# Optimization experiments

Measured on AMD Instinct MI355X. Metric: run time of the kernel, lower is better.

## Reference

```python
import jax, jax.numpy as jnp
import numpy as np

SQRT_HALF = np.float32(np.sqrt(0.5))
H_AX, W_AX = 2, 3


def _refl_idx(idx, r):
    # symmetric extension with edge repetition (np.pad mode='symmetric'),
    # identical to dtcwt's reflect(idx, -0.5, r-0.5). Static numpy computation.
    idx = np.mod(idx, 2 * r)
    return np.where(idx < r, idx, 2 * r - 1 - idx)


def _filt(X, h, axis):
    # Non-decimating 1-D filtering (dtcwt colfilter/rowfilter): symmetric pad by
    # len(h)//2, true convolution, 'valid' -> output same length as input.
    X = jnp.moveaxis(X, axis, -1)
    m = h.shape[0]
    m2 = m // 2
    L = X.shape[-1]
    Xp = jnp.pad(X, [(0, 0)] * (X.ndim - 1) + [(m2, m2)], mode='symmetric')
    out = sum(h[m - 1 - j] * Xp[..., j:j + L] for j in range(m))  # flip -> convolution
    return jnp.moveaxis(out, -1, axis)


def _dfilt(X, ha, hb, highpass, axis):
    # Decimate-by-2 dual-tree filtering (dtcwt coldfilt/rowdfilt).
    # ha filters one polyphase stream, hb the other; outputs are interleaved.
    X = jnp.moveaxis(X, axis, -1)
    r = X.shape[-1]
    assert r % 4 == 0, 'filtered dim must be a multiple of 4'
    m = ha.shape[0]
    m2 = m // 2
    xe = _refl_idx(np.arange(-m, r + m), r)        # symmetric-extended indices
    t = np.arange(5, r + 2 * m - 2, 4)             # 0-based MATLAB t = 6:4:r+2m-2
    hao, hae = ha[0::2], ha[1::2]
    hbo, hbe = hb[0::2], hb[1::2]

    def cv(rows, f):
        # 'valid' true convolution along gathered (stride-4) sample sequence
        A = X[..., rows]
        Lout = rows.shape[0] - m2 + 1              # == r // 4
        return sum(f[m2 - 1 - j] * A[..., j:j + Lout] for j in range(m2))

    ya = cv(xe[t - 1], hao) + cv(xe[t - 3], hae)
    yb = cv(xe[t], hbo) + cv(xe[t - 2], hbe)
    first, second = (yb, ya) if highpass else (ya, yb)
    Y = jnp.stack([first, second], axis=-1).reshape(X.shape[:-1] + (r // 2,))
    return jnp.moveaxis(Y, -1, axis)


def _q2c(y):
    # quads -> two complex subimages: p = (a+jb)/sqrt2, q = (d-jc)/sqrt2; z = p -/+ q
    a = y[..., 0::2, 0::2]
    b = y[..., 0::2, 1::2]
    c = y[..., 1::2, 0::2]
    d = y[..., 1::2, 1::2]
    z1 = ((a - d) * SQRT_HALF, (b + c) * SQRT_HALF)
    z2 = ((a + d) * SQRT_HALF, (b - c) * SQRT_HALF)
    return z1, z2


def _bands_to_yh(lh, hl, hh):
    # orientation order 15,45,75,105,135,165 degrees; output [N,C,6,H',W',2]
    (r15, i15), (r165, i165) = _q2c(lh)
    (r45, i45), (r135, i135) = _q2c(hh)
    (r75, i75), (r105, i105) = _q2c(hl)
    reals = jnp.stack([r15, r45, r75, r105, r135, r165], axis=2)
    imags = jnp.stack([i15, i45, i75, i105, i135, i165], axis=2)
    return jnp.stack([reals, imags], axis=-1)


def _dtcwt_fwd(x, h0o, h1o, h0a, h0b, h1a, h1b, J=3):
    # Level 1: non-decimating biorthogonal filters
    lo = _filt(x, h0o, W_AX)
    hi = _filt(x, h1o, W_AX)
    ll = _filt(lo, h0o, H_AX)
    yh = [_bands_to_yh(_filt(lo, h1o, H_AX),   # lh
                       _filt(hi, h0o, H_AX),   # hl
                       _filt(hi, h1o, H_AX))]  # hh
    # Levels 2..J: decimating qshift filters
    for _ in range(1, J):
        lo = _dfilt(ll, h0b, h0a, False, W_AX)
        hi = _dfilt(ll, h1b, h1a, True, W_AX)
        ll = _dfilt(lo, h0b, h0a, False, H_AX)
        yh.append(_bands_to_yh(_dfilt(lo, h1b, h1a, True, H_AX),
                               _dfilt(hi, h0b, h0a, False, H_AX),
                               _dfilt(hi, h1b, h1a, True, H_AX)))
    return (ll, *yh)


def setup_inputs() -> dict:
    key = jax.random.key(0)
    ks = jax.random.split(key, 5)
    x = jax.random.normal(ks[0], (4, 16, 512, 512), dtype=jnp.float32)

    def mk(k, n):
        h = jax.random.normal(k, (n,), dtype=jnp.float32)
        return h / jnp.linalg.norm(h)  # unit-norm to keep levels well scaled

    h0o = mk(ks[1], 5)
    h1o = mk(ks[2], 7)
    h0a = mk(ks[3], 10)
    h1a = mk(ks[4], 10)
    h0b = h0a[::-1]  # dual-tree property: tree-b = time-reversed tree-a
    h1b = h1a[::-1]
    return {'x': x, 'h0o': h0o, 'h1o': h1o, 'h0a': h0a, 'h0b': h0b,
            'h1a': h1a, 'h1b': h1b}


def reference(x, h0o, h1o, h0a, h0b, h1a, h1b):
    # Returns (yl, yh_level1, yh_level2, yh_level3)
    return _dtcwt_fwd(x, h0o, h1o, h0a, h0b, h1a, h1b, J=3)
```

## Files before the change

### kernel.cpp

```cpp
#include <hip/hip_runtime.h>

#define S1 512
#define NIMG 64

typedef float f4v __attribute__((ext_vector_type(4)));
typedef float f2v __attribute__((ext_vector_type(2)));

__device__ __forceinline__ int refl(int a, int L) {
    a = (a < 0) ? (-a - 1) : a;
    a = (a >= L) ? (2 * L - 1 - a) : a;
    return a;
}

__device__ __forceinline__ void st_nt_f4(float* p, float a, float b, float c, float d) {
    f4v w = {a, b, c, d};
    __builtin_nontemporal_store(w, (f4v*)p);
}
__device__ __forceinline__ void st_nt_f2(float* p, float a, float b) {
    f2v w = {a, b};
    __builtin_nontemporal_store(w, (f2v*)p);
}

__global__ __launch_bounds__(256) void k_level1(
    const float* __restrict__ x,
    const float* __restrict__ h0o_g, const float* __restrict__ h1o_g,
    float* __restrict__ ll1, float* __restrict__ yh0)
{
    __shared__ float xs[38 * 72];
    __shared__ float lo_s[38 * 68];
    __shared__ float hi_s[38 * 68];

    const int t  = threadIdx.x;
    const int c0 = blockIdx.x * 64;
    const int r0 = blockIdx.y * 64;
    const int n  = blockIdx.z;
    const float* __restrict__ xn  = x   + (size_t)n * (S1 * S1);
    float* __restrict__ lln       = ll1 + (size_t)n * (S1 * S1);
    float* __restrict__ yhn       = yh0 + (size_t)n * (6 * 256 * 256 * 2);

    float f0[5], f1[7];
#pragma unroll
    for (int i = 0; i < 5; ++i) f0[i] = h0o_g[i];
#pragma unroll
    for (int i = 0; i < 7; ++i) f1[i] = h1o_g[i];

    const float SQH = 0.70710678118654752440f;

    for (int h = 0; h < 2; ++h) {
        const int gr0 = r0 + 32 * h - 3;

        for (int l = t; l < 38 * 16; l += 256) {
            int rl = l >> 4, cf = l & 15;
            int ar = refl(gr0 + rl, S1);
            *(float4*)&xs[rl * 72 + 4 + 4 * cf] =
                *(const float4*)&xn[(size_t)ar * S1 + c0 + 4 * cf];
        }
        if (t < 76) {
            int rl = t >> 1, side = t & 1;
            const float* __restrict__ row = &xn[(size_t)refl(gr0 + rl, S1) * S1];
            int xc = side ? 68 : 0;
            int gc = side ? (c0 + 64) : (c0 - 4);
            if (gc >= 0 && gc + 3 < S1) {
                *(float4*)&xs[rl * 72 + xc] = *(const float4*)&row[gc];
            } else {
#pragma unroll
                for (int k = 0; k < 4; ++k)
                    xs[rl * 72 + xc + k] = row[refl(gc + k, S1)];
            }
        }
        __syncthreads();

        for (int l = t; l < 38 * 16; l += 256) {
            int rl = l >> 4, cg = l & 15;
            const float* p = &xs[rl * 72 + 4 * cg];
            float4 va = *(const float4*)p;
            float4 vb = *(const float4*)(p + 4);
            float4 vc = *(const float4*)(p + 8);
            float V[12] = {va.x, va.y, va.z, va.w, vb.x, vb.y, vb.z, vb.w,
                           vc.x, vc.y, vc.z, vc.w};
            float lov[4], hiv[4];
#pragma unroll
            for (int cc = 0; cc < 4; ++cc) {
                lov[cc] = f0[0]*V[cc+6] + f0[1]*V[cc+5] + f0[2]*V[cc+4]
                        + f0[3]*V[cc+3] + f0[4]*V[cc+2];
                hiv[cc] = f1[0]*V[cc+7] + f1[1]*V[cc+6] + f1[2]*V[cc+5]
                        + f1[3]*V[cc+4] + f1[4]*V[cc+3] + f1[5]*V[cc+2]
                        + f1[6]*V[cc+1];
            }
            *(float4*)&lo_s[rl * 68 + 4 * cg] = make_float4(lov[0], lov[1], lov[2], lov[3]);
            *(float4*)&hi_s[rl * 68 + 4 * cg] = make_float4(hiv[0], hiv[1], hiv[2], hiv[3]);
        }
        __syncthreads();

        {
            const int qi = t >> 4, cg = t & 15;
            float4 Lv[8];
            float llv[2][4], lhv[2][4], hlv[2][4], hhv[2][4];

#pragma unroll
            for (int j = 0; j < 8; ++j)
                Lv[j] = *(const float4*)&lo_s[(2 * qi + j) * 68 + 4 * cg];
            {
                const float* L = (const float*)Lv;
#pragma unroll
                for (int cc = 0; cc < 4; ++cc) {
                    float Lc[8];
#pragma unroll
                    for (int j = 0; j < 8; ++j) Lc[j] = L[4 * j + cc];
                    llv[0][cc] = f0[0]*Lc[5] + f0[1]*Lc[4] + f0[2]*Lc[3] + f0[3]*Lc[2] + f0[4]*Lc[1];
                    llv[1][cc] = f0[0]*Lc[6] + f0[1]*Lc[5] + f0[2]*Lc[4] + f0[3]*Lc[3] + f0[4]*Lc[2];
                    lhv[0][cc] = f1[0]*Lc[6] + f1[1]*Lc[5] + f1[2]*Lc[4] + f1[3]*Lc[3]
                               + f1[4]*Lc[2] + f1[5]*Lc[1] + f1[6]*Lc[0];
                    lhv[1][cc] = f1[0]*Lc[7] + f1[1]*Lc[6] + f1[2]*Lc[5] + f1[3]*Lc[4]
                               + f1[4]*Lc[3] + f1[5]*Lc[2] + f1[6]*Lc[1];
                }
            }
#pragma unroll
            for (int j = 0; j < 8; ++j)
                Lv[j] = *(const float4*)&hi_s[(2 * qi + j) * 68 + 4 * cg];
            {
                const float* L = (const float*)Lv;
#pragma unroll
                for (int cc = 0; cc < 4; ++cc) {
                    float Lc[8];
#pragma unroll
                    for (int j = 0; j < 8; ++j) Lc[j] = L[4 * j + cc];
                    hlv[0][cc] = f0[0]*Lc[5] + f0[1]*Lc[4] + f0[2]*Lc[3] + f0[3]*Lc[2] + f0[4]*Lc[1];
                    hlv[1][cc] = f0[0]*Lc[6] + f0[1]*Lc[5] + f0[2]*Lc[4] + f0[3]*Lc[3] + f0[4]*Lc[2];
                    hhv[0][cc] = f1[0]*Lc[6] + f1[1]*Lc[5] + f1[2]*Lc[4] + f1[3]*Lc[3]
                               + f1[4]*Lc[2] + f1[5]*Lc[1] + f1[6]*Lc[0];
                    hhv[1][cc] = f1[0]*Lc[7] + f1[1]*Lc[6] + f1[2]*Lc[5] + f1[3]*Lc[4]
                               + f1[4]*Lc[3] + f1[5]*Lc[2] + f1[6]*Lc[1];
                }
            }

            const int oy = r0 + 32 * h + 2 * qi, ox = c0 + 4 * cg;
            *(float4*)&lln[(size_t)oy * S1 + ox] =
                make_float4(llv[0][0], llv[0][1], llv[0][2], llv[0][3]);
            *(float4*)&lln[(size_t)(oy + 1) * S1 + ox] =
                make_float4(llv[1][0], llv[1][1], llv[1][2], llv[1][3]);

            const int i2 = (r0 >> 1) + 16 * h + qi, j2 = (c0 >> 1) + 2 * cg;
            const size_t bs = 256 * 256 * 2;
            float* __restrict__ p = yhn + ((size_t)i2 * 256 + j2) * 2;
#define ST_Z1(P, X0, X1) st_nt_f4((P), (X0[0]-X1[1])*SQH, (X0[1]+X1[0])*SQH, \
                                       (X0[2]-X1[3])*SQH, (X0[3]+X1[2])*SQH)
#define ST_Z2(P, X0, X1) st_nt_f4((P), (X0[0]+X1[1])*SQH, (X0[1]-X1[0])*SQH, \
                                       (X0[2]+X1[3])*SQH, (X0[3]-X1[2])*SQH)
            ST_Z1(p + 0 * bs, lhv[0], lhv[1]);
            ST_Z1(p + 1 * bs, hhv[0], hhv[1]);
            ST_Z1(p + 2 * bs, hlv[0], hlv[1]);
            ST_Z2(p + 3 * bs, hlv[0], hlv[1]);
            ST_Z2(p + 4 * bs, hhv[0], hhv[1]);
            ST_Z2(p + 5 * bs, lhv[0], lhv[1]);
#undef ST_Z1
#undef ST_Z2
        }
        __syncthreads();
    }
}

__global__ __launch_bounds__(256) void k_dfilt(
    const float* __restrict__ X, const int r,
    const float* __restrict__ h0a_g, const float* __restrict__ h0b_g,
    const float* __restrict__ h1a_g, const float* __restrict__ h1b_g,
    float* __restrict__ llo, float* __restrict__ yh)
{
    __shared__ float Xc[16 * 84];
    __shared__ float lo_s[80 * 36];
    __shared__ float hi_s[80 * 36];

    const int t  = threadIdx.x;
    const int x0 = blockIdx.x * 32;
    const int y0 = blockIdx.y * 32;
    const int n  = blockIdx.z;
    const float* __restrict__ Xn = X + (size_t)n * r * r;
    const int cb = 2 * x0 - 8, rb = 2 * y0 - 8;

    float fa0[10], fb0[10], fa1[10], fb1[10];
#pragma unroll
    for (int i = 0; i < 10; ++i) {
        fa0[i] = h0a_g[i]; fb0[i] = h0b_g[i];
        fa1[i] = h1a_g[i]; fb1[i] = h1b_g[i];
    }

    for (int c = 0; c < 5; ++c) {
        const int rbase = rb + 16 * c;
        {
            int rl = t >> 4, cf = t & 15;
            int ar = refl(rbase + rl, r);
            *(float4*)&Xc[rl * 84 + 8 + 4 * cf] =
                *(const float4*)&Xn[(size_t)ar * r + (cb + 8) + 4 * cf];
        }
        if (t < 64) {
            int rl = t >> 2, q = t & 3;
            const float* __restrict__ row = &Xn[(size_t)refl(rbase + rl, r) * r];
            int xc = (q < 2) ? (4 * q) : (72 + 4 * (q - 2));
            int gc = cb + xc;
            if (gc >= 0 && gc + 3 < r) {
                *(float4*)&Xc[rl * 84 + xc] = *(const float4*)&row[gc];
            } else {
#pragma unroll
                for (int k = 0; k < 4; ++k)
                    Xc[rl * 84 + xc + k] = row[refl(gc + k, r)];
            }
        }
        __syncthreads();

        {
            int rl = t >> 4, cp = t & 15;
            const float* p = &Xc[rl * 84 + 4 * cp];
            float V[20];
#pragma unroll
            for (int j = 0; j < 5; ++j) {
                float4 v = *(const float4*)(p + 4 * j);
                V[4*j+0] = v.x; V[4*j+1] = v.y; V[4*j+2] = v.z; V[4*j+3] = v.w;
            }
            float lo_e = 0.f, lo_o = 0.f, hi_e = 0.f, hi_o = 0.f;
#pragma unroll
            for (int k = 0; k < 10; ++k) {
                float ve = V[18 - 2 * k], vo = V[19 - 2 * k];
                lo_e += fb0[k] * ve;
                lo_o += fa0[k] * vo;
                hi_e += fa1[k] * vo;
                hi_o += fb1[k] * ve;
            }
            const int row = 16 * c + (t >> 4);
            *(float2*)&lo_s[row * 36 + 2 * cp] = make_float2(lo_e, lo_o);
            *(float2*)&hi_s[row * 36 + 2 * cp] = make_float2(hi_e, hi_o);
        }
        __syncthreads();
    }

    {
        const int qi = t >> 4, cg = t & 15;
        float2 Lv[20];
        float llq[2][2], lhq[2][2], hlq[2][2], hhq[2][2];

#pragma unroll
        for (int j = 0; j < 20; ++j)
            Lv[j] = *(const float2*)&lo_s[(4 * qi + j) * 36 + 2 * cg];
        {
            const float* L = (const float*)Lv;
#pragma unroll
            for (int cc = 0; cc < 2; ++cc) {
                float e0 = 0.f, o0 = 0.f, e1 = 0.f, o1 = 0.f;
#pragma unroll
                for (int k = 0; k < 10; ++k) {
                    float le = L[(18 - 2 * k) * 2 + cc], lo = L[(19 - 2 * k) * 2 + cc];
                    e0 += fb0[k] * le;
                    o0 += fa0[k] * lo;
                    e1 += fa1[k] * lo;
                    o1 += fb1[k] * le;
                }
                llq[0][cc] = e0; llq[1][cc] = o0;
                lhq[0][cc] = e1; lhq[1][cc] = o1;
            }
        }
#pragma unroll
        for (int j = 0; j < 20; ++j)
            Lv[j] = *(const float2*)&hi_s[(4 * qi + j) * 36 + 2 * cg];
        {
            const float* L = (const float*)Lv;
#pragma unroll
            for (int cc = 0; cc < 2; ++cc) {
                float e0 = 0.f, o0 = 0.f, e1 = 0.f, o1 = 0.f;
#pragma unroll
                for (int k = 0; k < 10; ++k) {
                    float he = L[(18 - 2 * k) * 2 + cc], ho = L[(19 - 2 * k) * 2 + cc];
                    e0 += fb0[k] * he;
                    o0 += fa0[k] * ho;
                    e1 += fa1[k] * ho;
                    o1 += fb1[k] * he;
                }
                hlq[0][cc] = e0; hlq[1][cc] = o0;
                hhq[0][cc] = e1; hhq[1][cc] = o1;
            }
        }

        const int R = r >> 1, R2 = r >> 2;
        const int oy = y0 + 2 * qi, ox = x0 + 2 * cg;
        *(float2*)&llo[((size_t)n * R + oy) * R + ox]     = make_float2(llq[0][0], llq[0][1]);
        *(float2*)&llo[((size_t)n * R + oy + 1) * R + ox] = make_float2(llq[1][0], llq[1][1]);

        const float SQH = 0.70710678118654752440f;
        const int i2 = (y0 >> 1) + qi, j2 = (x0 >> 1) + cg;
        const size_t bs = (size_t)R2 * R2 * 2;
        float* __restrict__ p = yh + (size_t)n * 6 * bs + ((size_t)i2 * R2 + j2) * 2;
        st_nt_f2(p + 0 * bs, (lhq[0][0] - lhq[1][1]) * SQH, (lhq[0][1] + lhq[1][0]) * SQH);
        st_nt_f2(p + 1 * bs, (hhq[0][0] - hhq[1][1]) * SQH, (hhq[0][1] + hhq[1][0]) * SQH);
        st_nt_f2(p + 2 * bs, (hlq[0][0] - hlq[1][1]) * SQH, (hlq[0][1] + hlq[1][0]) * SQH);
        st_nt_f2(p + 3 * bs, (hlq[0][0] + hlq[1][1]) * SQH, (hlq[0][1] - hlq[1][0]) * SQH);
        st_nt_f2(p + 4 * bs, (hhq[0][0] + hhq[1][1]) * SQH, (hhq[0][1] - hhq[1][0]) * SQH);
        st_nt_f2(p + 5 * bs, (lhq[0][0] + lhq[1][1]) * SQH, (lhq[0][1] - lhq[1][0]) * SQH);
    }
}

extern "C" void kernel_launch(void* const* d_in, const int* in_sizes, int n_in,
                              void* d_out, int out_size, void* d_ws, size_t ws_size,
                              hipStream_t stream) {
    const float* x   = (const float*)d_in[0];
    const float* h0o = (const float*)d_in[1];
    const float* h1o = (const float*)d_in[2];
    const float* h0a = (const float*)d_in[3];
    const float* h0b = (const float*)d_in[4];
    const float* h1a = (const float*)d_in[5];
    const float* h1b = (const float*)d_in[6];

    float* out = (float*)d_out;
    float* ll3 = out;
    float* yh0 = out + 1048576;
    float* yh1 = out + 51380224;
    float* yh2 = out + 63963136;

    float* ll1 = (float*)d_ws;
    float* ll2 = ll1 + 16777216;

    k_level1<<<dim3(8, 8, NIMG), 256, 0, stream>>>(x, h0o, h1o, ll1, yh0);
    k_dfilt<<<dim3(8, 8, NIMG), 256, 0, stream>>>(ll1, 512, h0a, h0b, h1a, h1b, ll2, yh1);
    k_dfilt<<<dim3(4, 4, NIMG), 256, 0, stream>>>(ll2, 256, h0a, h0b, h1a, h1b, ll3, yh2);
}
```

Before: 376.4 us.

## Prefetch next input tile into registers to overlap global loads with compute

In both the level-1 kernel and the decimating filter kernel, the next row chunk's global loads are issued into registers before the current chunk is computed, then written to shared memory at the start of the next iteration. This hides global-memory latency behind the filtering arithmetic and removes one trailing barrier in the level-1 kernel. It raises register pressure, which may reduce occupancy.

```diff
diff --git a/kernel.cpp b/kernel.cpp
--- a/kernel.cpp
+++ b/kernel.cpp
@@ -46,26 +46,49 @@
 
     const float SQH = 0.70710678118654752440f;
 
+    float4 pre0, pre1, pre2, preh;
+
+#pragma unroll
     for (int h = 0; h < 2; ++h) {
         const int gr0 = r0 + 32 * h - 3;
 
-        for (int l = t; l < 38 * 16; l += 256) {
-            int rl = l >> 4, cf = l & 15;
-            int ar = refl(gr0 + rl, S1);
-            *(float4*)&xs[rl * 72 + 4 + 4 * cf] =
-                *(const float4*)&xn[(size_t)ar * S1 + c0 + 4 * cf];
-        }
-        if (t < 76) {
-            int rl = t >> 1, side = t & 1;
-            const float* __restrict__ row = &xn[(size_t)refl(gr0 + rl, S1) * S1];
-            int xc = side ? 68 : 0;
-            int gc = side ? (c0 + 64) : (c0 - 4);
-            if (gc >= 0 && gc + 3 < S1) {
-                *(float4*)&xs[rl * 72 + xc] = *(const float4*)&row[gc];
-            } else {
-#pragma unroll
-                for (int k = 0; k < 4; ++k)
-                    xs[rl * 72 + xc + k] = row[refl(gc + k, S1)];
+        if (h == 0) {
+            for (int l = t; l < 38 * 16; l += 256) {
+                int rl = l >> 4, cf = l & 15;
+                int ar = refl(gr0 + rl, S1);
+                *(float4*)&xs[rl * 72 + 4 + 4 * cf] =
+                    *(const float4*)&xn[(size_t)ar * S1 + c0 + 4 * cf];
+            }
+            if (t < 76) {
+                int rl = t >> 1, side = t & 1;
+                const float* __restrict__ row = &xn[(size_t)refl(gr0 + rl, S1) * S1];
+                int xc = side ? 68 : 0;
+                int gc = side ? (c0 + 64) : (c0 - 4);
+                if (gc >= 0 && gc + 3 < S1) {
+                    *(float4*)&xs[rl * 72 + xc] = *(const float4*)&row[gc];
+                } else {
+#pragma unroll
+                    for (int k = 0; k < 4; ++k)
+                        xs[rl * 72 + xc + k] = row[refl(gc + k, S1)];
+                }
+            }
+        } else {
+            {
+                int rl = t >> 4, cf = t & 15;
+                *(float4*)&xs[rl * 72 + 4 + 4 * cf] = pre0;
+            }
+            {
+                int l = t + 256, rl = l >> 4, cf = l & 15;
+                *(float4*)&xs[rl * 72 + 4 + 4 * cf] = pre1;
+            }
+            if (t < 96) {
+                int l = t + 512, rl = l >> 4, cf = l & 15;
+                *(float4*)&xs[rl * 72 + 4 + 4 * cf] = pre2;
+            }
+            if (t < 76) {
+                int rl = t >> 1, side = t & 1;
+                int xc = side ? 68 : 0;
+                *(float4*)&xs[rl * 72 + xc] = preh;
             }
         }
         __syncthreads();
@@ -91,6 +114,39 @@
             *(float4*)&hi_s[rl * 68 + 4 * cg] = make_float4(hiv[0], hiv[1], hiv[2], hiv[3]);
         }
         __syncthreads();
+
+        if (h == 0) {
+            const int g1 = r0 + 32 - 3;
+            {
+                int rl = t >> 4, cf = t & 15;
+                int ar = refl(g1 + rl, S1);
+                pre0 = *(const float4*)&xn[(size_t)ar * S1 + c0 + 4 * cf];
+            }
+            {
+                int l = t + 256, rl = l >> 4, cf = l & 15;
+                int ar = refl(g1 + rl, S1);
+                pre1 = *(const float4*)&xn[(size_t)ar * S1 + c0 + 4 * cf];
+            }
+            if (t < 96) {
+                int l = t + 512, rl = l >> 4, cf = l & 15;
+                int ar = refl(g1 + rl, S1);
+                pre2 = *(const float4*)&xn[(size_t)ar * S1 + c0 + 4 * cf];
+            }
+            if (t < 76) {
+                int rl = t >> 1, side = t & 1;
+                const float* __restrict__ row = &xn[(size_t)refl(g1 + rl, S1) * S1];
+                int gc = side ? (c0 + 64) : (c0 - 4);
+                if (gc >= 0 && gc + 3 < S1) {
+                    preh = *(const float4*)&row[gc];
+                } else {
+                    float tmp[4];
+#pragma unroll
+                    for (int k = 0; k < 4; ++k)
+                        tmp[k] = row[refl(gc + k, S1)];
+                    preh = make_float4(tmp[0], tmp[1], tmp[2], tmp[3]);
+                }
+            }
+        }
 
         {
             const int qi = t >> 4, cg = t & 15;
@@ -156,7 +212,7 @@
 #undef ST_Z1
 #undef ST_Z2
         }
-        __syncthreads();
+        if (h == 0) __syncthreads();
     }
 }
 
@@ -184,13 +240,14 @@
         fa1[i] = h1a_g[i]; fb1[i] = h1b_g[i];
     }
 
-    for (int c = 0; c < 5; ++c) {
+    float4 creg, hreg;
+
+    auto load_chunk = [&](int c) {
         const int rbase = rb + 16 * c;
         {
             int rl = t >> 4, cf = t & 15;
             int ar = refl(rbase + rl, r);
-            *(float4*)&Xc[rl * 84 + 8 + 4 * cf] =
-                *(const float4*)&Xn[(size_t)ar * r + (cb + 8) + 4 * cf];
+            creg = *(const float4*)&Xn[(size_t)ar * r + (cb + 8) + 4 * cf];
         }
         if (t < 64) {
             int rl = t >> 2, q = t & 3;
@@ -198,14 +255,32 @@
             int xc = (q < 2) ? (4 * q) : (72 + 4 * (q - 2));
             int gc = cb + xc;
             if (gc >= 0 && gc + 3 < r) {
-                *(float4*)&Xc[rl * 84 + xc] = *(const float4*)&row[gc];
+                hreg = *(const float4*)&row[gc];
             } else {
+                float tmp[4];
 #pragma unroll
                 for (int k = 0; k < 4; ++k)
-                    Xc[rl * 84 + xc + k] = row[refl(gc + k, r)];
-            }
+                    tmp[k] = row[refl(gc + k, r)];
+                hreg = make_float4(tmp[0], tmp[1], tmp[2], tmp[3]);
+            }
+        }
+    };
+
+    load_chunk(0);
+
+    for (int c = 0; c < 5; ++c) {
+        {
+            int rl = t >> 4, cf = t & 15;
+            *(float4*)&Xc[rl * 84 + 8 + 4 * cf] = creg;
+        }
+        if (t < 64) {
+            int rl = t >> 2, q = t & 3;
+            int xc = (q < 2) ? (4 * q) : (72 + 4 * (q - 2));
+            *(float4*)&Xc[rl * 84 + xc] = hreg;
         }
         __syncthreads();
+
+        if (c < 4) load_chunk(c + 1);
 
         {
             int rl = t >> 4, cp = t & 15;
@@ -225,7 +300,7 @@
                 hi_e += fa1[k] * vo;
                 hi_o += fb1[k] * ve;
             }
-            const int row = 16 * c + (t >> 4);
+            const int row = 16 * c + rl;
             *(float2*)&lo_s[row * 36 + 2 * cp] = make_float2(lo_e, lo_o);
             *(float2*)&hi_s[row * 36 + 2 * cp] = make_float2(hi_e, hi_o);
         }
```

New measurement: 363.7 us. 3.4% less time.
